# Optimization experiments

Measured on AMD Instinct MI355X. Metric: run time of the kernel, lower is better.

The kernel has to match this reference:

```python
import jax, jax.numpy as jnp
import numpy as np

LEN_HIS = 20   # q_len_his: sliding-window history length
DIM_C = 4      # dim_c
H = 64         # GRU hidden = final_mlp_hidden_width
D = 36         # global_graph_width(32) + goal(2) + action(2)
N = 32768      # total timesteps across many episodes


def setup_inputs() -> dict:
    key = jax.random.key(0)
    ks = jax.random.split(key, 8)
    emb = jax.random.normal(ks[0], (N, D), jnp.float32)
    dones = (jax.random.uniform(ks[1], (N, 1)) < 0.02).astype(jnp.int32)
    s = lambda k, shape, fan: jax.random.normal(k, shape, jnp.float32) / np.sqrt(fan).astype(np.float32)
    return {
        "embeddings": emb,
        "W_ih": s(ks[2], (3 * H, D), D),
        "W_hh": s(ks[3], (3 * H, H), H),
        "b_ih": jnp.zeros((3 * H,), jnp.float32),
        "b_hh": jnp.zeros((3 * H,), jnp.float32),
        "W1": s(ks[4], (H, H), H),
        "b1": jnp.zeros((H,), jnp.float32),
        "W2": s(ks[5], (DIM_C, H), H),
        "b2": jnp.zeros((DIM_C,), jnp.float32),
        "dones": dones,
    }


def _his_calculate_c(embeddings, W_ih, W_hh, b_ih, b_hh, W1, b1, W2, b2, dones):
    """Batched/padded version of the ragged sliding-window GRU+MLP loop.

    For each timestep t, the torch code runs the GRU over
    embeddings[max(episode_start, t-L+1) : t+1] from a zero hidden state,
    then applies FinalPredMLP to the final hidden state.
    """
    n = embeddings.shape[0]
    done = dones[:, 0] != 0
    idx = jnp.arange(n)
    # episode_start[t] = (index of most recent done strictly before t) + 1, else 0
    prev_done = jnp.concatenate([jnp.zeros((1,), bool), done[:-1]])
    ep_start = jax.lax.cummax(jnp.where(prev_done, idx, 0))
    win_start = jnp.maximum(ep_start, idx - LEN_HIS + 1)            # [N]

    # padded windows: position l holds embeddings[t - (L-1) + l]
    gidx = idx[:, None] - (LEN_HIS - 1) + jnp.arange(LEN_HIS)[None, :]  # [N, L]
    valid = gidx >= win_start[:, None]                                   # [N, L]
    X = embeddings[jnp.clip(gidx, 0, n - 1)] * valid[..., None]          # [N, L, D]

    def cell(h, inp):
        x, v = inp                      # x: [N, D], v: [N]
        gi = x @ W_ih.T + b_ih          # [N, 3H]
        gh = h @ W_hh.T + b_hh          # [N, 3H]
        ir, iz, inn = jnp.split(gi, 3, axis=-1)
        hr, hz, hnn = jnp.split(gh, 3, axis=-1)
        r = jax.nn.sigmoid(ir + hr)
        z = jax.nn.sigmoid(iz + hz)
        ncand = jnp.tanh(inn + r * hnn)
        h_new = (1.0 - z) * ncand + z * h
        return jnp.where(v[:, None], h_new, h), None

    h0 = jnp.zeros((n, H), embeddings.dtype)
    hT, _ = jax.lax.scan(cell, h0, (jnp.swapaxes(X, 0, 1), valid.T))  # [N, H]

    # FinalPredMLP: Linear(H,H) -> ReLU -> Linear(H, dim_c)
    hid = jax.nn.relu(hT @ W1.T + b1)
    return hid @ W2.T + b2              # [N, dim_c]


def reference(embeddings, W_ih, W_hh, b_ih, b_hh, W1, b1, W2, b2, dones):
    return _his_calculate_c(embeddings, W_ih, W_hh, b_ih, b_hh, W1, b1, W2, b2, dones)
```

## Files before the change

kernel.cpp:

```cpp
#include <hip/hip_runtime.h>

#define NT 32768
#define DI 36
#define HH 64
#define LH 20
#define TPB 16
#define NROW 35
#define SGH 200
#define EMBS 40

#define NLOG2E -1.4426950408889634f
#define TLOG2E 2.8853900817779268f

#define UNION_OFF  14000
#define SMEM_BYTES 19600

typedef __attribute__((ext_vector_type(8))) short bf16x8;
typedef __attribute__((ext_vector_type(8))) _Float16 f16x8;
typedef __attribute__((ext_vector_type(4))) float f32x4;
typedef __attribute__((ext_vector_type(4))) int int4v;
union frag_cast { int4v i4; bf16x8 h8; };
union fh_cast { int4v i4; f16x8 h8; };

__device__ __forceinline__ unsigned f2u(float f) { union { float f; unsigned u; } x; x.f = f; return x.u; }
__device__ __forceinline__ float u2f(unsigned u) { union { float f; unsigned u; } x; x.u = u; return x.f; }
__device__ __forceinline__ unsigned short f2bf_rne(float f) {
    union { float f; unsigned u; } x; x.f = f;
    unsigned r = x.u + 0x7FFFu + ((x.u >> 16) & 1u);
    return (unsigned short)(r >> 16);
}
__device__ __forceinline__ unsigned pk2h(float a, float b) {
    auto h = __builtin_amdgcn_cvt_pkrtz(a, b);
    union { decltype(h) v; unsigned u; } x; x.v = h; return x.u;
}

__device__ __forceinline__ void gate4(const f32x4 aR, const f32x4 aZ,
                                      const f32x4 aI, const f32x4 aN,
                                      const bool valid, float* hh) {
    float dR[4], dZ[4], dN[4], rv[4], zv[4], iv[4];
#pragma unroll
    for (int e = 0; e < 4; ++e) dR[e] = 1.f + __builtin_amdgcn_exp2f(aR[e]);
#pragma unroll
    for (int e = 0; e < 4; ++e) dZ[e] = 1.f + __builtin_amdgcn_exp2f(aZ[e]);
    {
        const float pa = dR[0] * dR[1], pb = dR[2] * dR[3];
        const float rp = __builtin_amdgcn_rcpf(pa * pb);
        const float ia = rp * pb, ib = rp * pa;
        rv[0] = ia * dR[1]; rv[1] = ia * dR[0];
        rv[2] = ib * dR[3]; rv[3] = ib * dR[2];
    }
    {
        const float pa = dZ[0] * dZ[1], pb = dZ[2] * dZ[3];
        const float rp = __builtin_amdgcn_rcpf(pa * pb);
        const float ia = rp * pb, ib = rp * pa;
        zv[0] = ia * dZ[1]; zv[1] = ia * dZ[0];
        zv[2] = ib * dZ[3]; zv[3] = ib * dZ[2];
    }
#pragma unroll
    for (int e = 0; e < 4; ++e)
        dN[e] = 1.f + __builtin_amdgcn_exp2f(fmaf(rv[e], aN[e], aI[e]));
    {
        const float pa = dN[0] * dN[1], pb = dN[2] * dN[3];
        const float rp = __builtin_amdgcn_rcpf(pa * pb);
        const float ia = rp * pb, ib = rp * pa;
        iv[0] = ia * dN[1]; iv[1] = ia * dN[0];
        iv[2] = ib * dN[3]; iv[3] = ib * dN[2];
    }
#pragma unroll
    for (int e = 0; e < 4; ++e) {
        const float nc = fmaf(-2.f, iv[e], 1.f);
        const float hn = fmaf(zv[e], hh[e] - nc, nc);
        hh[e] = valid ? hn : hh[e];
    }
}

__global__ __launch_bounds__(64) void prep_kernel(
    const float* __restrict__ W_ih, const float* __restrict__ W_hh,
    const float* __restrict__ W1, int4v* __restrict__ wfrag)
{
    const int b = (int)blockIdx.x;
    const int l = (int)threadIdx.x;
    unsigned short e[8];
    if (b < 72) {
        const int set = b / 24, fb = b % 24;
        const int mt = fb >> 1, kt = fb & 1;
        const int m = mt * 16 + (l & 15);
        const float sc = ((mt >> 2) < 2) ? NLOG2E : TLOG2E;
        const int k0 = kt * 32 + (l >> 4) * 8;
#pragma unroll
        for (int jj = 0; jj < 8; ++jj) {
            const int k = k0 + jj;
            if (set == 2) {
                e[jj] = f2bf_rne(W_hh[(size_t)m * HH + k] * sc);
            } else {
                const float v = (k < DI) ? W_ih[(size_t)m * DI + k] * sc : 0.f;
                const unsigned u = f2u(v);
                if (set == 0) e[jj] = (unsigned short)(u >> 16);
                else          e[jj] = (unsigned short)(f2u(v - u2f(u & 0xFFFF0000u)) >> 16);
            }
        }
    } else {
        const int bb = b - 72;
        const bool is_lo = bb >= 8;
        const int f = bb & 7;
        const int mt = f >> 1, kt = f & 1;
        const int m = mt * 16 + (l & 15);
        const int k0 = kt * 32 + (l >> 4) * 8;
#pragma unroll
        for (int jj = 0; jj < 8; ++jj) {
            const float v = W1[(size_t)m * HH + k0 + jj];
            const unsigned u = f2u(v);
            if (!is_lo) e[jj] = (unsigned short)(u >> 16);
            else        e[jj] = (unsigned short)(f2u(v - u2f(u & 0xFFFF0000u)) >> 16);
        }
    }
    int4v p;
    p.x = e[0] | ((unsigned)e[1] << 16); p.y = e[2] | ((unsigned)e[3] << 16);
    p.z = e[4] | ((unsigned)e[5] << 16); p.w = e[6] | ((unsigned)e[7] << 16);
    wfrag[b * 64 + l] = p;
}

__global__ __launch_bounds__(128, 3) void gru_kernel(
    const float* __restrict__ emb, const int4v* __restrict__ wfrag,
    const float* __restrict__ b_ih, const float* __restrict__ b_hh,
    const float* __restrict__ b1, const float* __restrict__ W2,
    const float* __restrict__ b2, const int* __restrict__ dones,
    float* __restrict__ out)
{
    __shared__ __align__(16) char SMEM[SMEM_BYTES];
    unsigned short* const Sgh  = (unsigned short*)SMEM;
    unsigned short* const EmbH = (unsigned short*)(SMEM + UNION_OFF);
    unsigned short* const EmbL = EmbH + NROW * EMBS;
    unsigned short* const Hb   = (unsigned short*)(SMEM + UNION_OFF);
    float* const red = (float*)SMEM;

    const int tid = threadIdx.x;
    const int lane = tid & 63;
    const int W = tid >> 6;
    const int li = lane & 15;
    const int q = lane >> 4;
    const int mtw0 = 2 * W;
    const int blk = ((int)blockIdx.x & 7) * 256 + ((int)blockIdx.x >> 3);
    const int T0 = blk * TPB;

    int sfr;
    {
        const int tt = T0 + li;
        int off = (tt >= LH - 1) ? 0 : (LH - 1) - tt;
#pragma unroll
        for (int k = LH - 1; k >= 1; --k) {
            const int j = tt - k;
            const int jj = j < 0 ? 0 : j;
            const bool d = (j >= 0) && (dones[jj] != 0);
            if (d) off = LH - k;
        }
        sfr = off;
    }

    for (int i = tid; i < NROW * 9; i += 128) {
        const int r = i / 9, c = i - r * 9;
        int tt = T0 - (LH - 1) + r; tt = tt < 0 ? 0 : tt;
        const f32x4 v = *(const f32x4*)&emb[(size_t)tt * DI + 4 * c];
        const unsigned u0 = f2u(v[0]), u1 = f2u(v[1]);
        const unsigned u2 = f2u(v[2]), u3 = f2u(v[3]);
        uint2 ph, pl;
        ph.x = __builtin_amdgcn_perm(u1, u0, 0x07060302u);
        ph.y = __builtin_amdgcn_perm(u3, u2, 0x07060302u);
        const unsigned l0 = f2u(v[0] - u2f(u0 & 0xFFFF0000u));
        const unsigned l1 = f2u(v[1] - u2f(u1 & 0xFFFF0000u));
        const unsigned l2 = f2u(v[2] - u2f(u2 & 0xFFFF0000u));
        const unsigned l3 = f2u(v[3] - u2f(u3 & 0xFFFF0000u));
        pl.x = __builtin_amdgcn_perm(l1, l0, 0x07060302u);
        pl.y = __builtin_amdgcn_perm(l3, l2, 0x07060302u);
        *(uint2*)&EmbH[r * EMBS + 4 * c] = ph;
        *(uint2*)&EmbL[r * EMBS + 4 * c] = pl;
    }
    if (tid < NROW) {
        const uint2 z2 = {0u, 0u};
        *(uint2*)&EmbH[tid * EMBS + DI] = z2;
        *(uint2*)&EmbL[tid * EMBS + DI] = z2;
    }

    f32x4 biasI[3][2];
#pragma unroll
    for (int g = 0; g < 3; ++g) {
        const float sc = (g < 2) ? NLOG2E : TLOG2E;
#pragma unroll
        for (int ml = 0; ml < 2; ++ml) {
            const int jo = 16 * (mtw0 + ml) + 4 * q;
            const f32x4 bi = *(const f32x4*)&b_ih[64 * g + jo];
            if (g < 2) {
                const f32x4 bh = *(const f32x4*)&b_hh[64 * g + jo];
#pragma unroll
                for (int rr = 0; rr < 4; ++rr) biasI[g][ml][rr] = (bi[rr] + bh[rr]) * sc;
            } else {
#pragma unroll
                for (int rr = 0; rr < 4; ++rr) biasI[g][ml][rr] = bi[rr] * sc;
            }
        }
    }
    __syncthreads();

#pragma unroll
    for (int rt = 0; rt < 3; ++rt) {
        const int row = ((rt == 2) ? 19 : 16 * rt) + li;
        bf16x8 ebh0 = *(const bf16x8*)&EmbH[row * EMBS + 8 * q];
        bf16x8 ebl0 = *(const bf16x8*)&EmbL[row * EMBS + 8 * q];
        bf16x8 ebh1 = bf16x8{0, 0, 0, 0, 0, 0, 0, 0};
        bf16x8 ebl1 = bf16x8{0, 0, 0, 0, 0, 0, 0, 0};
        if (q == 0) {
            ebh1 = *(const bf16x8*)&EmbH[row * EMBS + 32];
            ebl1 = *(const bf16x8*)&EmbL[row * EMBS + 32];
        }
#pragma unroll
        for (int g = 0; g < 3; ++g)
#pragma unroll
            for (int ml = 0; ml < 2; ++ml) {
                const int fb = (4 * g + mtw0 + ml) * 2;
                frag_cast a0, a1, c0, c1;
                a0.i4 = wfrag[(fb + 0) * 64 + lane];
                a1.i4 = wfrag[(fb + 1) * 64 + lane];
                c0.i4 = wfrag[(24 + fb + 0) * 64 + lane];
                c1.i4 = wfrag[(24 + fb + 1) * 64 + lane];
                f32x4 a = biasI[g][ml];
                a = __builtin_amdgcn_mfma_f32_16x16x32_bf16(a0.h8, ebh0, a, 0, 0, 0);
                a = __builtin_amdgcn_mfma_f32_16x16x32_bf16(a1.h8, ebh1, a, 0, 0, 0);
                a = __builtin_amdgcn_mfma_f32_16x16x32_bf16(c0.h8, ebh0, a, 0, 0, 0);
                a = __builtin_amdgcn_mfma_f32_16x16x32_bf16(c1.h8, ebh1, a, 0, 0, 0);
                a = __builtin_amdgcn_mfma_f32_16x16x32_bf16(a0.h8, ebl0, a, 0, 0, 0);
                a = __builtin_amdgcn_mfma_f32_16x16x32_bf16(a1.h8, ebl1, a, 0, 0, 0);
                uint2 pk;
                pk.x = pk2h(a[0], a[1]);
                pk.y = pk2h(a[2], a[3]);
                *(uint2*)&Sgh[row * SGH + W * 96 + q * 24 + g * 8 + ml * 4] = pk;
            }
    }
    __syncthreads();

    bf16x8 whh[3][2][2];
#pragma unroll
    for (int g = 0; g < 3; ++g)
#pragma unroll
        for (int ml = 0; ml < 2; ++ml)
#pragma unroll
            for (int kt = 0; kt < 2; ++kt) {
                frag_cast c;
                c.i4 = wfrag[(48 + (4 * g + mtw0 + ml) * 2 + kt) * 64 + lane];
                whh[g][ml][kt] = c.h8;
            }
    f32x4 bnv[2];
#pragma unroll
    for (int ml = 0; ml < 2; ++ml) {
        const f32x4 b = *(const f32x4*)&b_hh[128 + 16 * (mtw0 + ml) + 4 * q];
#pragma unroll
        for (int rr = 0; rr < 4; ++rr) bnv[ml][rr] = b[rr] * TLOG2E;
    }
    const int gbase = W * 96 + q * 24;

    float h[2][4];
    {
        fh_cast cR, cZ, cI;
        cR.i4 = *(const int4v*)&Sgh[li * SGH + gbase + 0];
        cZ.i4 = *(const int4v*)&Sgh[li * SGH + gbase + 8];
        cI.i4 = *(const int4v*)&Sgh[li * SGH + gbase + 16];
        const bool valid = (0 >= sfr);
#pragma unroll
        for (int ml = 0; ml < 2; ++ml) {
            f32x4 aR, aZ, aI;
#pragma unroll
            for (int rr = 0; rr < 4; ++rr) {
                aR[rr] = (float)cR.h8[4 * ml + rr];
                aZ[rr] = (float)cZ.h8[4 * ml + rr];
                aI[rr] = (float)cI.h8[4 * ml + rr];
            }
            h[ml][0] = 0.f; h[ml][1] = 0.f; h[ml][2] = 0.f; h[ml][3] = 0.f;
            gate4(aR, aZ, aI, bnv[ml], valid, h[ml]);
            uint2 ph;
            ph.x = __builtin_amdgcn_perm(f2u(h[ml][1]), f2u(h[ml][0]), 0x07060302u);
            ph.y = __builtin_amdgcn_perm(f2u(h[ml][3]), f2u(h[ml][2]), 0x07060302u);
            *(uint2*)&Hb[li * 72 + 16 * (mtw0 + ml) + 4 * q] = ph;
        }
    }
    __syncthreads();

#pragma unroll 2
    for (int s = 1; s < LH; ++s) {
        const int rb = (s + 1) & 1;
        const bf16x8 bh0 = *(const bf16x8*)&Hb[rb * 1152 + li * 72 + 8 * q];
        const bf16x8 bh1 = *(const bf16x8*)&Hb[rb * 1152 + li * 72 + 32 + 8 * q];
        fh_cast cR, cZ, cI;
        const int gro = (li + s) * SGH + gbase;
        cR.i4 = *(const int4v*)&Sgh[gro + 0];
        cZ.i4 = *(const int4v*)&Sgh[gro + 8];
        cI.i4 = *(const int4v*)&Sgh[gro + 16];
        f32x4 aR[2], aZ[2], aI[2], aN[2];
#pragma unroll
        for (int ml = 0; ml < 2; ++ml) {
#pragma unroll
            for (int rr = 0; rr < 4; ++rr) {
                aR[ml][rr] = (float)cR.h8[4 * ml + rr];
                aZ[ml][rr] = (float)cZ.h8[4 * ml + rr];
                aI[ml][rr] = (float)cI.h8[4 * ml + rr];
            }
            aN[ml] = bnv[ml];
        }
#pragma unroll
        for (int ml = 0; ml < 2; ++ml) {
            aR[ml] = __builtin_amdgcn_mfma_f32_16x16x32_bf16(whh[0][ml][0], bh0, aR[ml], 0, 0, 0);
            aR[ml] = __builtin_amdgcn_mfma_f32_16x16x32_bf16(whh[0][ml][1], bh1, aR[ml], 0, 0, 0);
            aZ[ml] = __builtin_amdgcn_mfma_f32_16x16x32_bf16(whh[1][ml][0], bh0, aZ[ml], 0, 0, 0);
            aZ[ml] = __builtin_amdgcn_mfma_f32_16x16x32_bf16(whh[1][ml][1], bh1, aZ[ml], 0, 0, 0);
            aN[ml] = __builtin_amdgcn_mfma_f32_16x16x32_bf16(whh[2][ml][0], bh0, aN[ml], 0, 0, 0);
            aN[ml] = __builtin_amdgcn_mfma_f32_16x16x32_bf16(whh[2][ml][1], bh1, aN[ml], 0, 0, 0);
        }
        const bool valid = (s >= sfr);
#pragma unroll
        for (int ml = 0; ml < 2; ++ml) {
            gate4(aR[ml], aZ[ml], aI[ml], aN[ml], valid, h[ml]);
            uint2 ph;
            ph.x = __builtin_amdgcn_perm(f2u(h[ml][1]), f2u(h[ml][0]), 0x07060302u);
            ph.y = __builtin_amdgcn_perm(f2u(h[ml][3]), f2u(h[ml][2]), 0x07060302u);
            *(uint2*)&Hb[(s & 1) * 1152 + li * 72 + 16 * (mtw0 + ml) + 4 * q] = ph;
        }
        __syncthreads();
    }

#pragma unroll
    for (int ml = 0; ml < 2; ++ml) {
        const unsigned u0 = f2u(h[ml][0]), u1 = f2u(h[ml][1]);
        const unsigned u2 = f2u(h[ml][2]), u3 = f2u(h[ml][3]);
        const unsigned l0 = f2u(h[ml][0] - u2f(u0 & 0xFFFF0000u));
        const unsigned l1 = f2u(h[ml][1] - u2f(u1 & 0xFFFF0000u));
        const unsigned l2 = f2u(h[ml][2] - u2f(u2 & 0xFFFF0000u));
        const unsigned l3 = f2u(h[ml][3] - u2f(u3 & 0xFFFF0000u));
        uint2 pl;
        pl.x = __builtin_amdgcn_perm(l1, l0, 0x07060302u);
        pl.y = __builtin_amdgcn_perm(l3, l2, 0x07060302u);
        *(uint2*)&Hb[li * 72 + 16 * (mtw0 + ml) + 4 * q] = pl;
    }
    __syncthreads();
    const bf16x8 bh0 = *(const bf16x8*)&Hb[1152 + li * 72 + 8 * q];
    const bf16x8 bh1 = *(const bf16x8*)&Hb[1152 + li * 72 + 32 + 8 * q];
    const bf16x8 bl0 = *(const bf16x8*)&Hb[li * 72 + 8 * q];
    const bf16x8 bl1 = *(const bf16x8*)&Hb[li * 72 + 32 + 8 * q];

    float p0 = 0.f, p1 = 0.f, p2 = 0.f, p3 = 0.f;
#pragma unroll
    for (int ml = 0; ml < 2; ++ml) {
        frag_cast w1h0, w1h1, w1l0, w1l1;
        w1h0.i4 = wfrag[(72 + (mtw0 + ml) * 2 + 0) * 64 + lane];
        w1h1.i4 = wfrag[(72 + (mtw0 + ml) * 2 + 1) * 64 + lane];
        w1l0.i4 = wfrag[(80 + (mtw0 + ml) * 2 + 0) * 64 + lane];
        w1l1.i4 = wfrag[(80 + (mtw0 + ml) * 2 + 1) * 64 + lane];
        f32x4 a = *(const f32x4*)&b1[16 * (mtw0 + ml) + 4 * q];
        a = __builtin_amdgcn_mfma_f32_16x16x32_bf16(w1h0.h8, bh0, a, 0, 0, 0);
        a = __builtin_amdgcn_mfma_f32_16x16x32_bf16(w1h1.h8, bh1, a, 0, 0, 0);
        a = __builtin_amdgcn_mfma_f32_16x16x32_bf16(w1l0.h8, bh0, a, 0, 0, 0);
        a = __builtin_amdgcn_mfma_f32_16x16x32_bf16(w1l1.h8, bh1, a, 0, 0, 0);
        a = __builtin_amdgcn_mfma_f32_16x16x32_bf16(w1h0.h8, bl0, a, 0, 0, 0);
        a = __builtin_amdgcn_mfma_f32_16x16x32_bf16(w1h1.h8, bl1, a, 0, 0, 0);
        const float h0 = fmaxf(a[0], 0.f), h1 = fmaxf(a[1], 0.f);
        const float h2 = fmaxf(a[2], 0.f), h3 = fmaxf(a[3], 0.f);
        const int mo = 16 * (mtw0 + ml) + 4 * q;
        const f32x4 w0 = *(const f32x4*)&W2[0 * HH + mo];
        const f32x4 w1 = *(const f32x4*)&W2[1 * HH + mo];
        const f32x4 w2 = *(const f32x4*)&W2[2 * HH + mo];
        const f32x4 w3 = *(const f32x4*)&W2[3 * HH + mo];
        p0 += h0 * w0[0] + h1 * w0[1] + h2 * w0[2] + h3 * w0[3];
        p1 += h0 * w1[0] + h1 * w1[1] + h2 * w1[2] + h3 * w1[3];
        p2 += h0 * w2[0] + h1 * w2[1] + h2 * w2[2] + h3 * w2[3];
        p3 += h0 * w3[0] + h1 * w3[1] + h2 * w3[2] + h3 * w3[3];
    }
    p0 += __shfl_xor(p0, 16); p0 += __shfl_xor(p0, 32);
    p1 += __shfl_xor(p1, 16); p1 += __shfl_xor(p1, 32);
    p2 += __shfl_xor(p2, 16); p2 += __shfl_xor(p2, 32);
    p3 += __shfl_xor(p3, 16); p3 += __shfl_xor(p3, 32);
    const float pv = (q == 0) ? p0 : (q == 1) ? p1 : (q == 2) ? p2 : p3;
    red[W * 64 + li * 4 + q] = pv;
    __syncthreads();
    if (W == 0)
        out[(size_t)(T0 + li) * 4 + q] = red[li * 4 + q] + red[64 + li * 4 + q] + b2[q];
}

extern "C" void kernel_launch(void* const* d_in, const int* in_sizes, int n_in,
                              void* d_out, int out_size, void* d_ws, size_t ws_size,
                              hipStream_t stream) {
    const float* emb  = (const float*)d_in[0];
    const float* W_ih = (const float*)d_in[1];
    const float* W_hh = (const float*)d_in[2];
    const float* b_ih = (const float*)d_in[3];
    const float* b_hh = (const float*)d_in[4];
    const float* b1   = (const float*)d_in[6];
    const float* W2   = (const float*)d_in[7];
    const float* b2   = (const float*)d_in[8];
    const int*   dn   = (const int*)d_in[9];

    int4v* wfrag = (int4v*)d_ws;
    float* o = (float*)d_out;

    prep_kernel<<<88, 64, 0, stream>>>(W_ih, W_hh, (const float*)d_in[5], wfrag);
    gru_kernel<<<NT / TPB, 128, 0, stream>>>(emb, wfrag, b_ih, b_hh,
                                             b1, W2, b2, dn, o);
}
```

Before: 131.0 us.

## Enlarge blocks to 64 timesteps and keep input-projection gates in fp32 LDS

Each block now covers 64 timesteps with 512 threads (8 waves) instead of 16 timesteps with 128 threads. Waves share one embedding staging buffer of 83 rows, which cuts the redundant window overlap loads. Each wave keeps its W_ih fragments in registers, and the precomputed input gates are stored in LDS as fp32 instead of packed fp16, removing the conversions. The hidden-state exchange per step now uses a single per-column buffer with two block-wide barriers. This adds more barrier traffic over 512 threads and about 78KB of LDS per block, which can lower occupancy.

```diff
diff --git a/kernel.cpp b/kernel.cpp
--- a/kernel.cpp
+++ b/kernel.cpp
@@ -4,23 +4,21 @@
 #define DI 36
 #define HH 64
 #define LH 20
-#define TPB 16
-#define NROW 35
-#define SGH 200
+#define TPB 64
+#define NROW 83
+#define SGS 196
 #define EMBS 40
 
 #define NLOG2E -1.4426950408889634f
 #define TLOG2E 2.8853900817779268f
 
-#define UNION_OFF  14000
-#define SMEM_BYTES 19600
+#define UNION_OFF  65072
+#define SMEM_BYTES 78352
 
 typedef __attribute__((ext_vector_type(8))) short bf16x8;
-typedef __attribute__((ext_vector_type(8))) _Float16 f16x8;
 typedef __attribute__((ext_vector_type(4))) float f32x4;
 typedef __attribute__((ext_vector_type(4))) int int4v;
 union frag_cast { int4v i4; bf16x8 h8; };
-union fh_cast { int4v i4; f16x8 h8; };
 
 __device__ __forceinline__ unsigned f2u(float f) { union { float f; unsigned u; } x; x.f = f; return x.u; }
 __device__ __forceinline__ float u2f(unsigned u) { union { float f; unsigned u; } x; x.u = u; return x.f; }
@@ -28,10 +26,6 @@
     union { float f; unsigned u; } x; x.f = f;
     unsigned r = x.u + 0x7FFFu + ((x.u >> 16) & 1u);
     return (unsigned short)(r >> 16);
-}
-__device__ __forceinline__ unsigned pk2h(float a, float b) {
-    auto h = __builtin_amdgcn_cvt_pkrtz(a, b);
-    union { decltype(h) v; unsigned u; } x; x.v = h; return x.u;
 }
 
 __device__ __forceinline__ void gate4(const f32x4 aR, const f32x4 aZ,
@@ -120,7 +114,7 @@
     wfrag[b * 64 + l] = p;
 }
 
-__global__ __launch_bounds__(128, 3) void gru_kernel(
+__global__ __launch_bounds__(512, 4) void gru_kernel(
     const float* __restrict__ emb, const int4v* __restrict__ wfrag,
     const float* __restrict__ b_ih, const float* __restrict__ b_hh,
     const float* __restrict__ b1, const float* __restrict__ W2,
@@ -128,7 +122,7 @@
     float* __restrict__ out)
 {
     __shared__ __align__(16) char SMEM[SMEM_BYTES];
-    unsigned short* const Sgh  = (unsigned short*)SMEM;
+    float* const Sg = (float*)SMEM;
     unsigned short* const EmbH = (unsigned short*)(SMEM + UNION_OFF);
     unsigned short* const EmbL = EmbH + NROW * EMBS;
     unsigned short* const Hb   = (unsigned short*)(SMEM + UNION_OFF);
@@ -136,16 +130,18 @@
 
     const int tid = threadIdx.x;
     const int lane = tid & 63;
-    const int W = tid >> 6;
+    const int w = tid >> 6;
+    const int c = w & 3;
+    const int hf = w >> 2;
     const int li = lane & 15;
     const int q = lane >> 4;
-    const int mtw0 = 2 * W;
-    const int blk = ((int)blockIdx.x & 7) * 256 + ((int)blockIdx.x >> 3);
+    const int mtw0 = 2 * hf;
+    const int blk = ((int)blockIdx.x & 7) * 64 + ((int)blockIdx.x >> 3);
     const int T0 = blk * TPB;
 
     int sfr;
     {
-        const int tt = T0 + li;
+        const int tt = T0 + 16 * c + li;
         int off = (tt >= LH - 1) ? 0 : (LH - 1) - tt;
 #pragma unroll
         for (int k = LH - 1; k >= 1; --k) {
@@ -157,10 +153,10 @@
         sfr = off;
     }
 
-    for (int i = tid; i < NROW * 9; i += 128) {
-        const int r = i / 9, c = i - r * 9;
+    for (int i = tid; i < NROW * 9; i += 512) {
+        const int r = i / 9, cc = i - r * 9;
         int tt = T0 - (LH - 1) + r; tt = tt < 0 ? 0 : tt;
-        const f32x4 v = *(const f32x4*)&emb[(size_t)tt * DI + 4 * c];
+        const f32x4 v = *(const f32x4*)&emb[(size_t)tt * DI + 4 * cc];
         const unsigned u0 = f2u(v[0]), u1 = f2u(v[1]);
         const unsigned u2 = f2u(v[2]), u3 = f2u(v[3]);
         uint2 ph, pl;
@@ -172,8 +168,8 @@
         const unsigned l3 = f2u(v[3] - u2f(u3 & 0xFFFF0000u));
         pl.x = __builtin_amdgcn_perm(l1, l0, 0x07060302u);
         pl.y = __builtin_amdgcn_perm(l3, l2, 0x07060302u);
-        *(uint2*)&EmbH[r * EMBS + 4 * c] = ph;
-        *(uint2*)&EmbL[r * EMBS + 4 * c] = pl;
+        *(uint2*)&EmbH[r * EMBS + 4 * cc] = ph;
+        *(uint2*)&EmbL[r * EMBS + 4 * cc] = pl;
     }
     if (tid < NROW) {
         const uint2 z2 = {0u, 0u};
@@ -181,29 +177,40 @@
         *(uint2*)&EmbL[tid * EMBS + DI] = z2;
     }
 
-    f32x4 biasI[3][2];
+    bf16x8 aih[3][2], ail[3][2];
+#pragma unroll
+    for (int g = 0; g < 3; ++g)
+#pragma unroll
+        for (int kt = 0; kt < 2; ++kt) {
+            const int fb = (4 * g + c) * 2 + kt;
+            frag_cast a, b;
+            a.i4 = wfrag[(0 * 24 + fb) * 64 + lane];
+            b.i4 = wfrag[(1 * 24 + fb) * 64 + lane];
+            aih[g][kt] = a.h8; ail[g][kt] = b.h8;
+        }
+
+    const int joff = 16 * c + 4 * q;
+    f32x4 biasI[3];
 #pragma unroll
     for (int g = 0; g < 3; ++g) {
         const float sc = (g < 2) ? NLOG2E : TLOG2E;
-#pragma unroll
-        for (int ml = 0; ml < 2; ++ml) {
-            const int jo = 16 * (mtw0 + ml) + 4 * q;
-            const f32x4 bi = *(const f32x4*)&b_ih[64 * g + jo];
-            if (g < 2) {
-                const f32x4 bh = *(const f32x4*)&b_hh[64 * g + jo];
-#pragma unroll
-                for (int rr = 0; rr < 4; ++rr) biasI[g][ml][rr] = (bi[rr] + bh[rr]) * sc;
-            } else {
-#pragma unroll
-                for (int rr = 0; rr < 4; ++rr) biasI[g][ml][rr] = bi[rr] * sc;
-            }
+        const f32x4 bi = *(const f32x4*)&b_ih[64 * g + joff];
+        if (g < 2) {
+            const f32x4 bh = *(const f32x4*)&b_hh[64 * g + joff];
+#pragma unroll
+            for (int rr = 0; rr < 4; ++rr) biasI[g][rr] = (bi[rr] + bh[rr]) * sc;
+        } else {
+#pragma unroll
+            for (int rr = 0; rr < 4; ++rr) biasI[g][rr] = bi[rr] * sc;
         }
     }
     __syncthreads();
 
 #pragma unroll
     for (int rt = 0; rt < 3; ++rt) {
-        const int row = ((rt == 2) ? 19 : 16 * rt) + li;
+        const int tile = hf * 3 + rt;
+        const int row0 = (tile == 5) ? 67 : 16 * tile;
+        const int row = row0 + li;
         bf16x8 ebh0 = *(const bf16x8*)&EmbH[row * EMBS + 8 * q];
         bf16x8 ebl0 = *(const bf16x8*)&EmbL[row * EMBS + 8 * q];
         bf16x8 ebh1 = bf16x8{0, 0, 0, 0, 0, 0, 0, 0};
@@ -213,27 +220,16 @@
             ebl1 = *(const bf16x8*)&EmbL[row * EMBS + 32];
         }
 #pragma unroll
-        for (int g = 0; g < 3; ++g)
-#pragma unroll
-            for (int ml = 0; ml < 2; ++ml) {
-                const int fb = (4 * g + mtw0 + ml) * 2;
-                frag_cast a0, a1, c0, c1;
-                a0.i4 = wfrag[(fb + 0) * 64 + lane];
-                a1.i4 = wfrag[(fb + 1) * 64 + lane];
-                c0.i4 = wfrag[(24 + fb + 0) * 64 + lane];
-                c1.i4 = wfrag[(24 + fb + 1) * 64 + lane];
-                f32x4 a = biasI[g][ml];
-                a = __builtin_amdgcn_mfma_f32_16x16x32_bf16(a0.h8, ebh0, a, 0, 0, 0);
-                a = __builtin_amdgcn_mfma_f32_16x16x32_bf16(a1.h8, ebh1, a, 0, 0, 0);
-                a = __builtin_amdgcn_mfma_f32_16x16x32_bf16(c0.h8, ebh0, a, 0, 0, 0);
-                a = __builtin_amdgcn_mfma_f32_16x16x32_bf16(c1.h8, ebh1, a, 0, 0, 0);
-                a = __builtin_amdgcn_mfma_f32_16x16x32_bf16(a0.h8, ebl0, a, 0, 0, 0);
-                a = __builtin_amdgcn_mfma_f32_16x16x32_bf16(a1.h8, ebl1, a, 0, 0, 0);
-                uint2 pk;
-                pk.x = pk2h(a[0], a[1]);
-                pk.y = pk2h(a[2], a[3]);
-                *(uint2*)&Sgh[row * SGH + W * 96 + q * 24 + g * 8 + ml * 4] = pk;
-            }
+        for (int g = 0; g < 3; ++g) {
+            f32x4 a = biasI[g];
+            a = __builtin_amdgcn_mfma_f32_16x16x32_bf16(aih[g][0], ebh0, a, 0, 0, 0);
+            a = __builtin_amdgcn_mfma_f32_16x16x32_bf16(aih[g][1], ebh1, a, 0, 0, 0);
+            a = __builtin_amdgcn_mfma_f32_16x16x32_bf16(ail[g][0], ebh0, a, 0, 0, 0);
+            a = __builtin_amdgcn_mfma_f32_16x16x32_bf16(ail[g][1], ebh1, a, 0, 0, 0);
+            a = __builtin_amdgcn_mfma_f32_16x16x32_bf16(aih[g][0], ebl0, a, 0, 0, 0);
+            a = __builtin_amdgcn_mfma_f32_16x16x32_bf16(aih[g][1], ebl1, a, 0, 0, 0);
+            *(f32x4*)&Sg[row * SGS + 64 * g + joff] = a;
+        }
     }
     __syncthreads();
 
@@ -244,9 +240,9 @@
         for (int ml = 0; ml < 2; ++ml)
 #pragma unroll
             for (int kt = 0; kt < 2; ++kt) {
-                frag_cast c;
-                c.i4 = wfrag[(48 + (4 * g + mtw0 + ml) * 2 + kt) * 64 + lane];
-                whh[g][ml][kt] = c.h8;
+                frag_cast cc;
+                cc.i4 = wfrag[(48 + (4 * g + mtw0 + ml) * 2 + kt) * 64 + lane];
+                whh[g][ml][kt] = cc.h8;
             }
     f32x4 bnv[2];
 #pragma unroll
@@ -255,53 +251,43 @@
 #pragma unroll
         for (int rr = 0; rr < 4; ++rr) bnv[ml][rr] = b[rr] * TLOG2E;
     }
-    const int gbase = W * 96 + q * 24;
+    unsigned short* const Hbc = Hb + c * 1152;
 
     float h[2][4];
+    bf16x8 bh0, bh1;
     {
-        fh_cast cR, cZ, cI;
-        cR.i4 = *(const int4v*)&Sgh[li * SGH + gbase + 0];
-        cZ.i4 = *(const int4v*)&Sgh[li * SGH + gbase + 8];
-        cI.i4 = *(const int4v*)&Sgh[li * SGH + gbase + 16];
+        const float* gp = Sg + (16 * c + li) * SGS;
         const bool valid = (0 >= sfr);
 #pragma unroll
         for (int ml = 0; ml < 2; ++ml) {
-            f32x4 aR, aZ, aI;
-#pragma unroll
-            for (int rr = 0; rr < 4; ++rr) {
-                aR[rr] = (float)cR.h8[4 * ml + rr];
-                aZ[rr] = (float)cZ.h8[4 * ml + rr];
-                aI[rr] = (float)cI.h8[4 * ml + rr];
-            }
+            const int jo = 16 * (mtw0 + ml) + 4 * q;
+            const f32x4 aR = *(const f32x4*)(gp + jo);
+            const f32x4 aZ = *(const f32x4*)(gp + 64 + jo);
+            const f32x4 aI = *(const f32x4*)(gp + 128 + jo);
             h[ml][0] = 0.f; h[ml][1] = 0.f; h[ml][2] = 0.f; h[ml][3] = 0.f;
             gate4(aR, aZ, aI, bnv[ml], valid, h[ml]);
             uint2 ph;
             ph.x = __builtin_amdgcn_perm(f2u(h[ml][1]), f2u(h[ml][0]), 0x07060302u);
             ph.y = __builtin_amdgcn_perm(f2u(h[ml][3]), f2u(h[ml][2]), 0x07060302u);
-            *(uint2*)&Hb[li * 72 + 16 * (mtw0 + ml) + 4 * q] = ph;
-        }
-    }
-    __syncthreads();
-
-#pragma unroll 2
+            *(uint2*)&Hbc[li * 72 + jo] = ph;
+        }
+        __syncthreads();
+        bh0 = *(const bf16x8*)&Hbc[li * 72 + 8 * q];
+        bh1 = *(const bf16x8*)&Hbc[li * 72 + 32 + 8 * q];
+        __syncthreads();
+    }
+
+#pragma unroll 1
     for (int s = 1; s < LH; ++s) {
-        const int rb = (s + 1) & 1;
-        const bf16x8 bh0 = *(const bf16x8*)&Hb[rb * 1152 + li * 72 + 8 * q];
-        const bf16x8 bh1 = *(const bf16x8*)&Hb[rb * 1152 + li * 72 + 32 + 8 * q];
-        fh_cast cR, cZ, cI;
-        const int gro = (li + s) * SGH + gbase;
-        cR.i4 = *(const int4v*)&Sgh[gro + 0];
-        cZ.i4 = *(const int4v*)&Sgh[gro + 8];
-        cI.i4 = *(const int4v*)&Sgh[gro + 16];
+        const bool last = (s == LH - 1);
+        const float* gp = Sg + (16 * c + li + s) * SGS;
         f32x4 aR[2], aZ[2], aI[2], aN[2];
 #pragma unroll
         for (int ml = 0; ml < 2; ++ml) {
-#pragma unroll
-            for (int rr = 0; rr < 4; ++rr) {
-                aR[ml][rr] = (float)cR.h8[4 * ml + rr];
-                aZ[ml][rr] = (float)cZ.h8[4 * ml + rr];
-                aI[ml][rr] = (float)cI.h8[4 * ml + rr];
-            }
+            const int jo = 16 * (mtw0 + ml) + 4 * q;
+            aR[ml] = *(const f32x4*)(gp + jo);
+            aZ[ml] = *(const f32x4*)(gp + 64 + jo);
+            aI[ml] = *(const f32x4*)(gp + 128 + jo);
             aN[ml] = bnv[ml];
         }
 #pragma unroll
@@ -317,14 +303,32 @@
 #pragma unroll
         for (int ml = 0; ml < 2; ++ml) {
             gate4(aR[ml], aZ[ml], aI[ml], aN[ml], valid, h[ml]);
-            uint2 ph;
-            ph.x = __builtin_amdgcn_perm(f2u(h[ml][1]), f2u(h[ml][0]), 0x07060302u);
-            ph.y = __builtin_amdgcn_perm(f2u(h[ml][3]), f2u(h[ml][2]), 0x07060302u);
-            *(uint2*)&Hb[(s & 1) * 1152 + li * 72 + 16 * (mtw0 + ml) + 4 * q] = ph;
-        }
-        __syncthreads();
-    }
-
+            if (!last) {
+                uint2 ph;
+                ph.x = __builtin_amdgcn_perm(f2u(h[ml][1]), f2u(h[ml][0]), 0x07060302u);
+                ph.y = __builtin_amdgcn_perm(f2u(h[ml][3]), f2u(h[ml][2]), 0x07060302u);
+                *(uint2*)&Hbc[li * 72 + 16 * (mtw0 + ml) + 4 * q] = ph;
+            }
+        }
+        if (!last) {
+            __syncthreads();
+            bh0 = *(const bf16x8*)&Hbc[li * 72 + 8 * q];
+            bh1 = *(const bf16x8*)&Hbc[li * 72 + 32 + 8 * q];
+            __syncthreads();
+        }
+    }
+
+#pragma unroll
+    for (int ml = 0; ml < 2; ++ml) {
+        uint2 ph;
+        ph.x = __builtin_amdgcn_perm(f2u(h[ml][1]), f2u(h[ml][0]), 0x07060302u);
+        ph.y = __builtin_amdgcn_perm(f2u(h[ml][3]), f2u(h[ml][2]), 0x07060302u);
+        *(uint2*)&Hbc[li * 72 + 16 * (mtw0 + ml) + 4 * q] = ph;
+    }
+    __syncthreads();
+    const bf16x8 fh0 = *(const bf16x8*)&Hbc[li * 72 + 8 * q];
+    const bf16x8 fh1 = *(const bf16x8*)&Hbc[li * 72 + 32 + 8 * q];
+    __syncthreads();
 #pragma unroll
     for (int ml = 0; ml < 2; ++ml) {
         const unsigned u0 = f2u(h[ml][0]), u1 = f2u(h[ml][1]);
@@ -336,13 +340,11 @@
         uint2 pl;
         pl.x = __builtin_amdgcn_perm(l1, l0, 0x07060302u);
         pl.y = __builtin_amdgcn_perm(l3, l2, 0x07060302u);
-        *(uint2*)&Hb[li * 72 + 16 * (mtw0 + ml) + 4 * q] = pl;
-    }
-    __syncthreads();
-    const bf16x8 bh0 = *(const bf16x8*)&Hb[1152 + li * 72 + 8 * q];
-    const bf16x8 bh1 = *(const bf16x8*)&Hb[1152 + li * 72 + 32 + 8 * q];
-    const bf16x8 bl0 = *(const bf16x8*)&Hb[li * 72 + 8 * q];
-    const bf16x8 bl1 = *(const bf16x8*)&Hb[li * 72 + 32 + 8 * q];
+        *(uint2*)&Hbc[li * 72 + 16 * (mtw0 + ml) + 4 * q] = pl;
+    }
+    __syncthreads();
+    const bf16x8 fl0 = *(const bf16x8*)&Hbc[li * 72 + 8 * q];
+    const bf16x8 fl1 = *(const bf16x8*)&Hbc[li * 72 + 32 + 8 * q];
 
     float p0 = 0.f, p1 = 0.f, p2 = 0.f, p3 = 0.f;
 #pragma unroll
@@ -353,12 +355,12 @@
         w1l0.i4 = wfrag[(80 + (mtw0 + ml) * 2 + 0) * 64 + lane];
         w1l1.i4 = wfrag[(80 + (mtw0 + ml) * 2 + 1) * 64 + lane];
         f32x4 a = *(const f32x4*)&b1[16 * (mtw0 + ml) + 4 * q];
-        a = __builtin_amdgcn_mfma_f32_16x16x32_bf16(w1h0.h8, bh0, a, 0, 0, 0);
-        a = __builtin_amdgcn_mfma_f32_16x16x32_bf16(w1h1.h8, bh1, a, 0, 0, 0);
-        a = __builtin_amdgcn_mfma_f32_16x16x32_bf16(w1l0.h8, bh0, a, 0, 0, 0);
-        a = __builtin_amdgcn_mfma_f32_16x16x32_bf16(w1l1.h8, bh1, a, 0, 0, 0);
-        a = __builtin_amdgcn_mfma_f32_16x16x32_bf16(w1h0.h8, bl0, a, 0, 0, 0);
-        a = __builtin_amdgcn_mfma_f32_16x16x32_bf16(w1h1.h8, bl1, a, 0, 0, 0);
+        a = __builtin_amdgcn_mfma_f32_16x16x32_bf16(w1h0.h8, fh0, a, 0, 0, 0);
+        a = __builtin_amdgcn_mfma_f32_16x16x32_bf16(w1h1.h8, fh1, a, 0, 0, 0);
+        a = __builtin_amdgcn_mfma_f32_16x16x32_bf16(w1l0.h8, fh0, a, 0, 0, 0);
+        a = __builtin_amdgcn_mfma_f32_16x16x32_bf16(w1l1.h8, fh1, a, 0, 0, 0);
+        a = __builtin_amdgcn_mfma_f32_16x16x32_bf16(w1h0.h8, fl0, a, 0, 0, 0);
+        a = __builtin_amdgcn_mfma_f32_16x16x32_bf16(w1h1.h8, fl1, a, 0, 0, 0);
         const float h0 = fmaxf(a[0], 0.f), h1 = fmaxf(a[1], 0.f);
         const float h2 = fmaxf(a[2], 0.f), h3 = fmaxf(a[3], 0.f);
         const int mo = 16 * (mtw0 + ml) + 4 * q;
@@ -376,10 +378,11 @@
     p2 += __shfl_xor(p2, 16); p2 += __shfl_xor(p2, 32);
     p3 += __shfl_xor(p3, 16); p3 += __shfl_xor(p3, 32);
     const float pv = (q == 0) ? p0 : (q == 1) ? p1 : (q == 2) ? p2 : p3;
-    red[W * 64 + li * 4 + q] = pv;
-    __syncthreads();
-    if (W == 0)
-        out[(size_t)(T0 + li) * 4 + q] = red[li * 4 + q] + red[64 + li * 4 + q] + b2[q];
+    red[(c * 2 + hf) * 64 + li * 4 + q] = pv;
+    __syncthreads();
+    if (hf == 0)
+        out[(size_t)(T0 + 16 * c + li) * 4 + q] =
+            red[(c * 2) * 64 + li * 4 + q] + red[(c * 2 + 1) * 64 + li * 4 + q] + b2[q];
 }
 
 extern "C" void kernel_launch(void* const* d_in, const int* in_sizes, int n_in,
@@ -390,6 +393,7 @@
     const float* W_hh = (const float*)d_in[2];
     const float* b_ih = (const float*)d_in[3];
     const float* b_hh = (const float*)d_in[4];
+    const float* W1   = (const float*)d_in[5];
     const float* b1   = (const float*)d_in[6];
     const float* W2   = (const float*)d_in[7];
     const float* b2   = (const float*)d_in[8];
@@ -398,7 +402,7 @@
     int4v* wfrag = (int4v*)d_ws;
     float* o = (float*)d_out;
 
-    prep_kernel<<<88, 64, 0, stream>>>(W_ih, W_hh, (const float*)d_in[5], wfrag);
-    gru_kernel<<<NT / TPB, 128, 0, stream>>>(emb, wfrag, b_ih, b_hh,
+    prep_kernel<<<88, 64, 0, stream>>>(W_ih, W_hh, W1, wfrag);
+    gru_kernel<<<NT / TPB, 512, 0, stream>>>(emb, wfrag, b_ih, b_hh,
                                              b1, W2, b2, dn, o);
 }
```

Result: faster. 117.2 us (-10.5%).
